# Performance work log

Measured on AMD Instinct MI355X. Metric: run time of the kernel, lower is better.

## Reference

```python
import jax, jax.numpy as jnp
import numpy as np

N_NODES = 100000
N_EDGES = 3200000
NEG_SLOPE = 0.2  # PyG GATConv default leaky_relu slope


def gat_layer(x, src, dst, W, att_src, att_dst, bias, heads, out_ch, concat):
    N = x.shape[0]
    h = (x @ W).reshape(N, heads, out_ch)              # [N, H, C]
    a_src = jnp.sum(h * att_src[None], axis=-1)        # [N, H]
    a_dst = jnp.sum(h * att_dst[None], axis=-1)        # [N, H]
    e = jax.nn.leaky_relu(a_src[src] + a_dst[dst], NEG_SLOPE)  # [E, H]
    m = jax.ops.segment_max(e, dst, num_segments=N)    # segment softmax (stable)
    e = jnp.exp(e - m[dst])
    s = jax.ops.segment_sum(e, dst, num_segments=N)
    alpha = e / (s[dst] + 1e-16)                       # [E, H]
    msg = h[src] * alpha[:, :, None]                   # [E, H, C]
    out = jax.ops.segment_sum(msg, dst, num_segments=N)  # [N, H, C]
    out = out.reshape(N, heads * out_ch) if concat else out.mean(axis=1)
    return out + bias


def setup_inputs() -> dict:
    key = jax.random.key(0)
    ks = jax.random.split(key, 8)
    x = jax.random.normal(ks[0], (N_NODES, 512), dtype=jnp.float32)
    edge_index = jax.random.randint(ks[1], (2, N_EDGES), 0, N_NODES, dtype=jnp.int64)
    s1 = 1.0 / np.sqrt(512.0)
    s2 = 1.0 / np.sqrt(64.0)
    return {
        "x": x,
        "edge_index": edge_index,
        "W1": jax.random.normal(ks[2], (512, 64), dtype=jnp.float32) * s1,
        "att_src1": jax.random.normal(ks[3], (8, 8), dtype=jnp.float32) * s2,
        "att_dst1": jax.random.normal(ks[4], (8, 8), dtype=jnp.float32) * s2,
        "b1": jnp.zeros((64,), dtype=jnp.float32),
        "W2": jax.random.normal(ks[5], (64, 16), dtype=jnp.float32) * s2,
        "att_src2": jax.random.normal(ks[6], (1, 16), dtype=jnp.float32) * 0.25,
        "att_dst2": jax.random.normal(ks[7], (1, 16), dtype=jnp.float32) * 0.25,
        "b2": jnp.zeros((16,), dtype=jnp.float32),
    }


def reference(x, edge_index, W1, att_src1, att_dst1, b1, W2, att_src2, att_dst2, b2):
    N = x.shape[0]
    # add self-loops (PyG GATConv default) so every node has at least one edge
    loops = jnp.arange(N, dtype=edge_index.dtype)
    src = jnp.concatenate([edge_index[0], loops])
    dst = jnp.concatenate([edge_index[1], loops])
    # eval mode: dropout(p=0.6, training=False) is identity
    h = jax.nn.elu(gat_layer(x, src, dst, W1, att_src1, att_dst1, b1, 8, 8, True))
    z = gat_layer(h, src, dst, W2, att_src2, att_dst2, b2, 1, 16, False)
    return jax.nn.log_softmax(z, axis=1)
```

## Files before the change

### kernel.cpp

```cpp
#include <hip/hip_runtime.h>
#include <hip/hip_bf16.h>
#include <math.h>

#define LEAKY 0.2f
#define BSHIFT 7
#define NBUCK_MAX 1024
#define BCAP 6144
#define CHUNK 8192
#define CCAP 6656

typedef __attribute__((ext_vector_type(8))) short short8v;
typedef __attribute__((ext_vector_type(4))) float f32x4;

__device__ __forceinline__ unsigned pkbf(float a, float b) {
  __hip_bfloat162 t = __float22bfloat162_rn(make_float2(a, b));
  return *(unsigned*)&t;
}
__device__ __forceinline__ unsigned short f2bf(float f) {
  __hip_bfloat16 h = __float2bfloat16(f);
  return *(unsigned short*)&h;
}
__device__ __forceinline__ float bflo(unsigned u) { return __uint_as_float(u << 16); }
__device__ __forceinline__ float bfhi(unsigned u) { return __uint_as_float(u & 0xFFFF0000u); }

__global__ __launch_bounds__(256) void setup_kernel(
    const float* __restrict__ W1, unsigned short* __restrict__ w1t,
    int* __restrict__ bucketCursor) {
  int t = blockIdx.x * 256 + threadIdx.x;
  if (t < 64 * 512) {
    int k = t & 511, c = t >> 9;
    w1t[(size_t)c * 512 + k] = f2bf(W1[(size_t)k * 64 + c]);
  }
  if (t < NBUCK_MAX) bucketCursor[t] = t * BCAP;
}

__global__ __launch_bounds__(256) void binB_kernel(
    const int* __restrict__ src, const int* __restrict__ dst,
    int* __restrict__ bucketCursor, unsigned* __restrict__ ebuf,
    int E, int Etot, int NBUCK) {
  __shared__ unsigned sorted[CHUNK];
  __shared__ unsigned short sbk2[CHUNK];
  __shared__ int bcnt[NBUCK_MAX];
  __shared__ int bofs[NBUCK_MAX];
  __shared__ int bdel[NBUCK_MAX];
  __shared__ int bcur[NBUCK_MAX];
  __shared__ int wsum[256];
  const int t = threadIdx.x;
  const int c0 = blockIdx.x * CHUNK;
  const int cnt = min(CHUNK, Etot - c0);
  for (int i = t; i < NBUCK_MAX; i += 256) bcnt[i] = 0;
  __syncthreads();
  for (int i = t; i < cnt; i += 256) {
    int g = c0 + i;
    int d = (g < E) ? dst[g] : (g - E);
    atomicAdd(&bcnt[d >> BSHIFT], 1);
  }
  __syncthreads();
  {
    int b4 = t * 4;
    int e0 = bcnt[b4], e1 = bcnt[b4 + 1], e2 = bcnt[b4 + 2], e3 = bcnt[b4 + 3];
    int s = e0 + e1 + e2 + e3;
    wsum[t] = s;
    __syncthreads();
    for (int off = 1; off < 256; off <<= 1) {
      int u = (t >= off) ? wsum[t - off] : 0;
      __syncthreads();
      wsum[t] += u;
      __syncthreads();
    }
    int excl = wsum[t] - s;
    bofs[b4] = excl;
    bofs[b4 + 1] = excl + e0;
    bofs[b4 + 2] = excl + e0 + e1;
    bofs[b4 + 3] = excl + e0 + e1 + e2;
  }
  __syncthreads();
  for (int i = t; i < NBUCK; i += 256) {
    int c = bcnt[i];
    int r = c ? atomicAdd(&bucketCursor[i], c) : 0;
    bdel[i] = r - bofs[i];
    bcur[i] = 0;
  }
  __syncthreads();
  for (int i = t; i < cnt; i += 256) {
    int g = c0 + i;
    int s, d;
    if (g < E) { s = src[g]; d = dst[g]; } else { s = d = g - E; }
    int b = d >> BSHIFT;
    int pos = bofs[b] + atomicAdd(&bcur[b], 1);
    sorted[pos] = (unsigned)s | ((unsigned)(d & 127) << 20);
    sbk2[pos] = (unsigned short)b;
  }
  __syncthreads();
  for (int i = t; i < cnt; i += 256) {
    int b = sbk2[i];
    ebuf[bdel[b] + i] = sorted[i];
  }
}

__global__ __launch_bounds__(256) void binC_kernel(
    const unsigned* __restrict__ ebuf, const int* __restrict__ bucketCursor,
    int2* __restrict__ seg, int* __restrict__ esrc, int N) {
  __shared__ unsigned stage[CCAP];
  __shared__ int hist[128];
  __shared__ int sA[128];
  __shared__ int curs[128];
  const int t = threadIdx.x;
  const int b = blockIdx.x;
  const int lo = b * BCAP;
  const int cnt = bucketCursor[b] - lo;
  const int base = b << BSHIFT;
  if (t < 128) hist[t] = 0;
  __syncthreads();
  for (int i = t; i < cnt; i += 256) {
    unsigned p = ebuf[lo + i];
    stage[i] = p;
    atomicAdd(&hist[p >> 20], 1);
  }
  __syncthreads();
  int v = 0;
  if (t < 128) { v = hist[t]; sA[t] = v; }
  __syncthreads();
  for (int off = 1; off < 128; off <<= 1) {
    int u = 0;
    if (t < 128 && t >= off) u = sA[t - off];
    __syncthreads();
    if (t < 128) sA[t] += u;
    __syncthreads();
  }
  if (t < 128) {
    int excl = sA[t] - v;
    curs[t] = excl;
    if (base + t < N) seg[base + t] = make_int2(lo + excl, v);
  }
  __syncthreads();
  for (int i = t; i < cnt; i += 256) {
    unsigned p = stage[i];
    int pos = atomicAdd(&curs[p >> 20], 1);
    esrc[lo + pos] = (int)(p & 0xFFFFFu);
  }
}

__global__ __launch_bounds__(256) void gemm1_kernel(
    const float* __restrict__ x, const unsigned short* __restrict__ w1t,
    unsigned short* __restrict__ h1b, int M) {
  __shared__ __align__(16) unsigned short AsU[128][40];
  __shared__ __align__(16) unsigned short BtU[64][40];
  const int tid = threadIdx.x;
  const int m0 = blockIdx.x * 128;
  const int w = tid >> 6, lane = tid & 63;
  const int l15 = lane & 15, lhi = lane >> 4;

  f32x4 acc[2][4];
#pragma unroll
  for (int r = 0; r < 2; ++r)
#pragma unroll
    for (int t = 0; t < 4; ++t) acc[r][t] = (f32x4){0.f, 0.f, 0.f, 0.f};

  for (int k0 = 0; k0 < 512; k0 += 32) {
#pragma unroll
    for (int u = 0; u < 4; ++u) {
      int q = u * 256 + tid;
      int r = q >> 3, c4 = q & 7;
      int gm = m0 + r;
      float4 v = make_float4(0.f, 0.f, 0.f, 0.f);
      if (gm < M) v = *(const float4*)(x + (size_t)gm * 512 + k0 + c4 * 4);
      *(uint2*)&AsU[r][c4 * 4] = make_uint2(pkbf(v.x, v.y), pkbf(v.z, v.w));
    }
    {
      int c = tid >> 2, kb = (tid & 3) * 8;
      short8v v = *(const short8v*)(w1t + (size_t)c * 512 + k0 + kb);
      *(short8v*)&BtU[c][kb] = v;
    }
    __syncthreads();

    short8v a0 = *(const short8v*)&AsU[32 * w + l15][lhi * 8];
    short8v a1 = *(const short8v*)&AsU[32 * w + 16 + l15][lhi * 8];
#pragma unroll
    for (int t = 0; t < 4; ++t) {
      short8v b = *(const short8v*)&BtU[16 * t + l15][lhi * 8];
      acc[0][t] = __builtin_amdgcn_mfma_f32_16x16x32_bf16(a0, b, acc[0][t], 0, 0, 0);
      acc[1][t] = __builtin_amdgcn_mfma_f32_16x16x32_bf16(a1, b, acc[1][t], 0, 0, 0);
    }
    __syncthreads();
  }
#pragma unroll
  for (int rt = 0; rt < 2; ++rt) {
#pragma unroll
    for (int t = 0; t < 4; ++t) {
#pragma unroll
      for (int reg = 0; reg < 4; ++reg) {
        int gm = m0 + 32 * w + 16 * rt + 4 * lhi + reg;
        if (gm < M) h1b[(size_t)gm * 64 + 16 * t + l15] = f2bf(acc[rt][t][reg]);
      }
    }
  }
}

__global__ __launch_bounds__(256) void agg1_kernel(
    const int2* __restrict__ seg, const int* __restrict__ esrc,
    const unsigned short* __restrict__ h1b, const float* __restrict__ att_src,
    const float* __restrict__ att_dst, const float* __restrict__ b1,
    const float* __restrict__ W2, unsigned short* __restrict__ g2b, int N) {
  __shared__ float Ws[1024];
  {
    float4 v = ((const float4*)W2)[threadIdx.x & 255];
    *(float4*)&Ws[(threadIdx.x & 255) * 4] = v;
  }
  __syncthreads();
  int wid = (blockIdx.x * 256 + threadIdx.x) >> 6;
  int lane = threadIdx.x & 63;
  if (wid >= N) return;
  const int n = wid;
  const int eo = lane >> 3, q = lane & 7;
  float as[8], ad[8];
  {
    float4 t0 = *(const float4*)(att_src + 8 * q);
    float4 t1 = *(const float4*)(att_src + 8 * q + 4);
    as[0] = t0.x; as[1] = t0.y; as[2] = t0.z; as[3] = t0.w;
    as[4] = t1.x; as[5] = t1.y; as[6] = t1.z; as[7] = t1.w;
    t0 = *(const float4*)(att_dst + 8 * q);
    t1 = *(const float4*)(att_dst + 8 * q + 4);
    ad[0] = t0.x; ad[1] = t0.y; ad[2] = t0.z; ad[3] = t0.w;
    ad[4] = t1.x; ad[5] = t1.y; ad[6] = t1.z; ad[7] = t1.w;
  }
  float adn;
  {
    uint4 hv = *(const uint4*)(h1b + (size_t)n * 64 + 8 * q);
    adn = bflo(hv.x) * ad[0] + bfhi(hv.x) * ad[1] + bflo(hv.y) * ad[2] +
          bfhi(hv.y) * ad[3] + bflo(hv.z) * ad[4] + bfhi(hv.z) * ad[5] +
          bflo(hv.w) * ad[6] + bfhi(hv.w) * ad[7];
  }
  const int2 sg = seg[n];
  const int s0 = sg.x, s1 = sg.x + sg.y;
  float acc[8] = {0.f, 0.f, 0.f, 0.f, 0.f, 0.f, 0.f, 0.f};
  float psum = 0.f;
  for (int i = s0 + eo; i < s1; i += 8) {
    int s = esrc[i];
    uint4 hv = *(const uint4*)(h1b + (size_t)s * 64 + 8 * q);
    float g[8];
    g[0] = bflo(hv.x); g[1] = bfhi(hv.x); g[2] = bflo(hv.y); g[3] = bfhi(hv.y);
    g[4] = bflo(hv.z); g[5] = bfhi(hv.z); g[6] = bflo(hv.w); g[7] = bfhi(hv.w);
    float u = g[0] * as[0] + g[1] * as[1] + g[2] * as[2] + g[3] * as[3] +
              g[4] * as[4] + g[5] * as[5] + g[6] * as[6] + g[7] * as[7];
    float e = u + adn;
    e = e > 0.f ? e : LEAKY * e;
    float p = __expf(e);
#pragma unroll
    for (int j = 0; j < 8; ++j) acc[j] += p * g[j];
    psum += p;
  }
#pragma unroll
  for (int off = 8; off <= 32; off <<= 1) {
#pragma unroll
    for (int j = 0; j < 8; ++j) acc[j] += __shfl_xor(acc[j], off);
    psum += __shfl_xor(psum, off);
  }
  float inv = 1.0f / (psum + 1e-16f);
  float4 b0 = *(const float4*)(b1 + 8 * q);
  float4 b14 = *(const float4*)(b1 + 8 * q + 4);
  float bb[8] = {b0.x, b0.y, b0.z, b0.w, b14.x, b14.y, b14.z, b14.w};
  float o[8];
#pragma unroll
  for (int j = 0; j < 8; ++j) {
    float v = acc[j] * inv + bb[j];
    o[j] = v > 0.f ? v : expm1f(v);
  }
  float p0 = 0.f, p1 = 0.f;
#pragma unroll
  for (int j = 0; j < 8; ++j) {
    float2 wv = *(const float2*)&Ws[(8 * q + j) * 16 + 2 * eo];
    p0 += o[j] * wv.x;
    p1 += o[j] * wv.y;
  }
  p0 += __shfl_xor(p0, 1); p0 += __shfl_xor(p0, 2); p0 += __shfl_xor(p0, 4);
  p1 += __shfl_xor(p1, 1); p1 += __shfl_xor(p1, 2); p1 += __shfl_xor(p1, 4);
  if (q == 0)
    *(unsigned*)&g2b[(size_t)n * 16 + 2 * eo] = pkbf(p0, p1);
}

__global__ __launch_bounds__(256) void agg2_kernel(
    const int2* __restrict__ seg, const int* __restrict__ esrc,
    const unsigned short* __restrict__ g2b, const float* __restrict__ att_src,
    const float* __restrict__ att_dst, const float* __restrict__ b2,
    float* __restrict__ out, int N) {
  int wid = (blockIdx.x * 256 + threadIdx.x) >> 6;
  int lane = threadIdx.x & 63;
  if (wid >= N) return;
  const int n = wid;
  const int eo = lane >> 2, q = lane & 3;
  const float4 as4 = *(const float4*)(att_src + 4 * q);
  const float4 ad4 = *(const float4*)(att_dst + 4 * q);

  float adn;
  {
    uint2 gv = *(const uint2*)(g2b + (size_t)n * 16 + 4 * q);
    float un = bflo(gv.x) * ad4.x + bfhi(gv.x) * ad4.y +
               bflo(gv.y) * ad4.z + bfhi(gv.y) * ad4.w;
    un += __shfl_xor(un, 1);
    un += __shfl_xor(un, 2);
    adn = un;
  }

  const int2 sg = seg[n];
  const int s0 = sg.x, s1 = sg.x + sg.y;
  float a0 = 0.f, a1 = 0.f, a2 = 0.f, a3 = 0.f, psum = 0.f;
  for (int i = s0 + eo; i < s1; i += 16) {
    int s = esrc[i];
    uint2 gv = *(const uint2*)(g2b + (size_t)s * 16 + 4 * q);
    float g0 = bflo(gv.x), g1 = bfhi(gv.x), g2v = bflo(gv.y), g3 = bfhi(gv.y);
    float u = g0 * as4.x + g1 * as4.y + g2v * as4.z + g3 * as4.w;
    u += __shfl_xor(u, 1);
    u += __shfl_xor(u, 2);
    float e = u + adn;
    e = e > 0.f ? e : LEAKY * e;
    float p = __expf(e);
    a0 += p * g0; a1 += p * g1; a2 += p * g2v; a3 += p * g3;
    psum += p;
  }
#pragma unroll
  for (int off = 4; off <= 32; off <<= 1) {
    a0 += __shfl_xor(a0, off);
    a1 += __shfl_xor(a1, off);
    a2 += __shfl_xor(a2, off);
    a3 += __shfl_xor(a3, off);
    psum += __shfl_xor(psum, off);
  }

  float inv = 1.0f / (psum + 1e-16f);
  float z0 = a0 * inv + b2[4 * q + 0];
  float z1 = a1 * inv + b2[4 * q + 1];
  float z2 = a2 * inv + b2[4 * q + 2];
  float z3 = a3 * inv + b2[4 * q + 3];
  float mx = fmaxf(fmaxf(z0, z1), fmaxf(z2, z3));
  mx = fmaxf(mx, __shfl_xor(mx, 1));
  mx = fmaxf(mx, __shfl_xor(mx, 2));
  float ex = __expf(z0 - mx) + __expf(z1 - mx) + __expf(z2 - mx) + __expf(z3 - mx);
  ex += __shfl_xor(ex, 1);
  ex += __shfl_xor(ex, 2);
  float lse = mx + logf(ex);
  if (eo == 0)
    *(float4*)(out + (size_t)n * 16 + 4 * q) =
        make_float4(z0 - lse, z1 - lse, z2 - lse, z3 - lse);
}

extern "C" void kernel_launch(void* const* d_in, const int* in_sizes, int n_in,
                              void* d_out, int out_size, void* d_ws, size_t ws_size,
                              hipStream_t stream) {
  const float* x        = (const float*)d_in[0];
  const int*   ei       = (const int*)d_in[1];
  const float* W1       = (const float*)d_in[2];
  const float* att_src1 = (const float*)d_in[3];
  const float* att_dst1 = (const float*)d_in[4];
  const float* b1       = (const float*)d_in[5];
  const float* W2       = (const float*)d_in[6];
  const float* att_src2 = (const float*)d_in[7];
  const float* att_dst2 = (const float*)d_in[8];
  const float* b2       = (const float*)d_in[9];
  float* out = (float*)d_out;

  const int N = in_sizes[0] / 512;
  const int E = in_sizes[1] / 2;
  const int Etot = E + N;
  const int NBUCK = (N + 127) >> BSHIFT;

  char* base = (char*)d_ws;
  size_t off = 0;
  auto alloc = [&](size_t bytes) { void* p = base + off; off = (off + bytes + 15) & ~(size_t)15; return p; };
  unsigned short* h1b = (unsigned short*)alloc((size_t)N * 64 * 2);
  unsigned short* g2b = (unsigned short*)alloc((size_t)N * 16 * 2);
  int*      esrc  = (int*)alloc((size_t)NBUCK * BCAP * 4);
  unsigned* ebuf  = (unsigned*)alloc((size_t)NBUCK * BCAP * 4);
  int2*     seg   = (int2*)alloc((size_t)N * 8);
  int* bucketCursor = (int*)alloc(NBUCK_MAX * 4);
  unsigned short* w1t = (unsigned short*)alloc(64 * 512 * 2);

  const int* srcI = ei;
  const int* dstI = ei + E;

  setup_kernel<<<128, 256, 0, stream>>>(W1, w1t, bucketCursor);
  binB_kernel<<<(Etot + CHUNK - 1) / CHUNK, 256, 0, stream>>>(
      srcI, dstI, bucketCursor, ebuf, E, Etot, NBUCK);
  binC_kernel<<<NBUCK, 256, 0, stream>>>(ebuf, bucketCursor, seg, esrc, N);

  gemm1_kernel<<<(N + 127) / 128, 256, 0, stream>>>(x, w1t, h1b, N);
  agg1_kernel<<<(N * 64 + 255) / 256, 256, 0, stream>>>(
      seg, esrc, h1b, att_src1, att_dst1, b1, W2, g2b, N);

  agg2_kernel<<<(N * 64 + 255) / 256, 256, 0, stream>>>(
      seg, esrc, g2b, att_src2, att_dst2, b2, out, N);
}
```

Measured before the change: 277.6 us.

## Simplify edge binning scatter and prefetch next GEMM tile into registers

The binning kernel drops the in-block prefix scan and the sorted LDS staging. Each edge now scatters straight to its global bucket slot using a per-bucket reservation plus an LDS atomic cursor. The src/dst reads happen once in the first pass instead of twice. The layer-1 GEMM prefetches the next k-tile of x and W1 into registers while MFMAs run on the current tile, to hide global load latency. The tradeoff is that global writes in binning become less coalesced and edge order within buckets becomes nondeterministic.

After: 259.2 us. 6.6% less time.

```diff
diff --git a/kernel.cpp b/kernel.cpp
--- a/kernel.cpp
+++ b/kernel.cpp
@@ -38,13 +38,11 @@
     const int* __restrict__ src, const int* __restrict__ dst,
     int* __restrict__ bucketCursor, unsigned* __restrict__ ebuf,
     int E, int Etot, int NBUCK) {
-  __shared__ unsigned sorted[CHUNK];
-  __shared__ unsigned short sbk2[CHUNK];
+  __shared__ unsigned stage[CHUNK];
+  __shared__ unsigned short sbk[CHUNK];
   __shared__ int bcnt[NBUCK_MAX];
-  __shared__ int bofs[NBUCK_MAX];
-  __shared__ int bdel[NBUCK_MAX];
+  __shared__ int bres[NBUCK_MAX];
   __shared__ int bcur[NBUCK_MAX];
-  __shared__ int wsum[256];
   const int t = threadIdx.x;
   const int c0 = blockIdx.x * CHUNK;
   const int cnt = min(CHUNK, Etot - c0);
@@ -52,49 +50,23 @@
   __syncthreads();
   for (int i = t; i < cnt; i += 256) {
     int g = c0 + i;
-    int d = (g < E) ? dst[g] : (g - E);
+    int s, d;
+    if (g < E) { s = src[g]; d = dst[g]; } else { s = d = g - E; }
+    stage[i] = (unsigned)s | ((unsigned)(d & 127) << 20);
+    sbk[i] = (unsigned short)(d >> BSHIFT);
     atomicAdd(&bcnt[d >> BSHIFT], 1);
-  }
-  __syncthreads();
-  {
-    int b4 = t * 4;
-    int e0 = bcnt[b4], e1 = bcnt[b4 + 1], e2 = bcnt[b4 + 2], e3 = bcnt[b4 + 3];
-    int s = e0 + e1 + e2 + e3;
-    wsum[t] = s;
-    __syncthreads();
-    for (int off = 1; off < 256; off <<= 1) {
-      int u = (t >= off) ? wsum[t - off] : 0;
-      __syncthreads();
-      wsum[t] += u;
-      __syncthreads();
-    }
-    int excl = wsum[t] - s;
-    bofs[b4] = excl;
-    bofs[b4 + 1] = excl + e0;
-    bofs[b4 + 2] = excl + e0 + e1;
-    bofs[b4 + 3] = excl + e0 + e1 + e2;
   }
   __syncthreads();
   for (int i = t; i < NBUCK; i += 256) {
     int c = bcnt[i];
-    int r = c ? atomicAdd(&bucketCursor[i], c) : 0;
-    bdel[i] = r - bofs[i];
+    bres[i] = c ? atomicAdd(&bucketCursor[i], c) : 0;
     bcur[i] = 0;
   }
   __syncthreads();
   for (int i = t; i < cnt; i += 256) {
-    int g = c0 + i;
-    int s, d;
-    if (g < E) { s = src[g]; d = dst[g]; } else { s = d = g - E; }
-    int b = d >> BSHIFT;
-    int pos = bofs[b] + atomicAdd(&bcur[b], 1);
-    sorted[pos] = (unsigned)s | ((unsigned)(d & 127) << 20);
-    sbk2[pos] = (unsigned short)b;
-  }
-  __syncthreads();
-  for (int i = t; i < cnt; i += 256) {
-    int b = sbk2[i];
-    ebuf[bdel[b] + i] = sorted[i];
+    int b = sbk[i];
+    int slot = bres[b] + atomicAdd(&bcur[b], 1);
+    ebuf[slot] = stage[i];
   }
 }
 
@@ -157,22 +129,43 @@
 #pragma unroll
     for (int t = 0; t < 4; ++t) acc[r][t] = (f32x4){0.f, 0.f, 0.f, 0.f};
 
+  float4 pv[4];
+  short8v pw;
+  const int cB = tid >> 2, kbB = (tid & 3) * 8;
+
+#pragma unroll
+  for (int u = 0; u < 4; ++u) {
+    int q = u * 256 + tid;
+    int r = q >> 3, c4 = q & 7;
+    int gm = m0 + r;
+    pv[u] = (gm < M) ? *(const float4*)(x + (size_t)gm * 512 + c4 * 4)
+                     : make_float4(0.f, 0.f, 0.f, 0.f);
+  }
+  pw = *(const short8v*)(w1t + (size_t)cB * 512 + kbB);
+
   for (int k0 = 0; k0 < 512; k0 += 32) {
 #pragma unroll
     for (int u = 0; u < 4; ++u) {
       int q = u * 256 + tid;
       int r = q >> 3, c4 = q & 7;
-      int gm = m0 + r;
-      float4 v = make_float4(0.f, 0.f, 0.f, 0.f);
-      if (gm < M) v = *(const float4*)(x + (size_t)gm * 512 + k0 + c4 * 4);
-      *(uint2*)&AsU[r][c4 * 4] = make_uint2(pkbf(v.x, v.y), pkbf(v.z, v.w));
+      *(uint2*)&AsU[r][c4 * 4] =
+          make_uint2(pkbf(pv[u].x, pv[u].y), pkbf(pv[u].z, pv[u].w));
     }
-    {
-      int c = tid >> 2, kb = (tid & 3) * 8;
-      short8v v = *(const short8v*)(w1t + (size_t)c * 512 + k0 + kb);
-      *(short8v*)&BtU[c][kb] = v;
+    *(short8v*)&BtU[cB][kbB] = pw;
+    __syncthreads();
+
+    if (k0 + 32 < 512) {
+      int k1 = k0 + 32;
+#pragma unroll
+      for (int u = 0; u < 4; ++u) {
+        int q = u * 256 + tid;
+        int r = q >> 3, c4 = q & 7;
+        int gm = m0 + r;
+        pv[u] = (gm < M) ? *(const float4*)(x + (size_t)gm * 512 + k1 + c4 * 4)
+                         : make_float4(0.f, 0.f, 0.f, 0.f);
+      }
+      pw = *(const short8v*)(w1t + (size_t)cB * 512 + k1 + kbB);
     }
-    __syncthreads();
 
     short8v a0 = *(const short8v*)&AsU[32 * w + l15][lhi * 8];
     short8v a1 = *(const short8v*)&AsU[32 * w + 16 + l15][lhi * 8];
```
